# Kernel optimization log

Measured on AMD Instinct MI355X. Metric: run time of the kernel, lower is better.

Reference implementation:

```python
import jax, jax.numpy as jnp
import numpy as np

NEG_SLOPE = 0.2  # PyG GATConv default leaky_relu slope


def _gat_conv(x, src, dst, W, a_src, a_dst, b, num_nodes):
    # Linear transform: [N, F_out]
    h = x @ W
    # Per-node attention halves (heads=1): [N]
    alpha_s = h @ a_src
    alpha_d = h @ a_dst
    # Per-edge raw score for edge j->i: a_src.h_j + a_dst.h_i
    e = jax.nn.leaky_relu(alpha_s[src] + alpha_d[dst], NEG_SLOPE)
    # Softmax over edges grouped by destination node (numerically stable)
    m = jax.ops.segment_max(e, dst, num_segments=num_nodes)
    ex = jnp.exp(e - m[dst])
    denom = jax.ops.segment_sum(ex, dst, num_segments=num_nodes)
    coef = ex / denom[dst]
    # Attention-weighted aggregation of source features into destinations
    out = jax.ops.segment_sum(h[src] * coef[:, None], dst, num_segments=num_nodes)
    return out + b


def setup_inputs() -> dict:
    key = jax.random.key(0)
    ks = jax.random.split(key, 12)
    N, F_in, F_hid, F_out, E = 100000, 128, 64, 40, 1600000
    x = jax.random.normal(ks[0], (N, F_in), dtype=jnp.float32)
    edge_index = jax.random.randint(ks[1], (2, E), 0, N, dtype=jnp.int64)
    g = lambda k, shape, fan: jax.random.normal(k, shape, dtype=jnp.float32) * (1.0 / np.sqrt(fan))
    return {
        "x": x,
        "edge_index": edge_index,
        "W1": g(ks[2], (F_in, F_hid), F_in),
        "a_src1": g(ks[3], (F_hid,), F_hid),
        "a_dst1": g(ks[4], (F_hid,), F_hid),
        "b1": jnp.zeros((F_hid,), dtype=jnp.float32),
        "W2": g(ks[5], (F_hid, F_out), F_hid),
        "a_src2": g(ks[6], (F_out,), F_out),
        "a_dst2": g(ks[7], (F_out,), F_out),
        "b2": jnp.zeros((F_out,), dtype=jnp.float32),
    }


def reference(x, edge_index, W1, a_src1, a_dst1, b1, W2, a_src2, a_dst2, b2):
    N = x.shape[0]
    # PyG GATConv adds self loops by default
    loops = jnp.arange(N, dtype=edge_index.dtype)
    src = jnp.concatenate([edge_index[0], loops])
    dst = jnp.concatenate([edge_index[1], loops])
    h = _gat_conv(x, src, dst, W1, a_src1, a_dst1, b1, N)
    h = jax.nn.relu(h)
    # dropout p=0.5 is inactive in eval mode
    h = _gat_conv(h, src, dst, W2, a_src2, a_dst2, b2, N)
    return jax.nn.log_softmax(h, axis=-1)
```

## Files before the change

### kernel.cpp

```cpp
#include <hip/hip_runtime.h>
#include <math.h>


constexpr int F_IN = 128;
constexpr int F_H  = 64;
constexpr int F_O  = 40;
constexpr int NBMAX = 512;
constexpr int CHUNK = 8192;

__device__ __forceinline__ unsigned f2bf(float f) {
    unsigned u = __float_as_uint(f);
    return (u + 0x7FFFu + ((u >> 16) & 1u)) >> 16;
}
__device__ __forceinline__ float bflo(unsigned u) { return __uint_as_float(u << 16); }
__device__ __forceinline__ float bfhi(unsigned u) { return __uint_as_float(u & 0xFFFF0000u); }


__global__ __launch_bounds__(256) void k_binA(const int* __restrict__ dsts,
                                              int* __restrict__ bcnt,
                                              int E, int Et, int NB) {
    __shared__ int hist[NBMAX];
    for (int i = threadIdx.x; i < NB; i += 256) hist[i] = 0;
    __syncthreads();
    int e0 = blockIdx.x * 2048;
#pragma unroll
    for (int it = 0; it < 8; ++it) {
        int e = e0 + it * 256 + threadIdx.x;
        if (e < Et) {
            int d = (e < E) ? dsts[e] : (e - E);
            atomicAdd(&hist[d >> 8], 1);
        }
    }
    __syncthreads();
    for (int i = threadIdx.x; i < NB; i += 256) {
        int c = hist[i];
        if (c) atomicAdd(&bcnt[i], c);
    }
}

__global__ __launch_bounds__(NBMAX) void k_binB(const int* __restrict__ bcnt,
                                                int* __restrict__ bbase,
                                                int* __restrict__ bcur,
                                                int* __restrict__ rp,
                                                int NB, int N, int Et) {
    __shared__ int sc[NBMAX];
    int t = threadIdx.x;
    int v = (t < NB) ? bcnt[t] : 0;
    sc[t] = v; __syncthreads();
    int x = v;
    for (int o = 1; o < NBMAX; o <<= 1) {
        int y = (t >= o) ? sc[t - o] : 0;
        __syncthreads();
        x += y;
        sc[t] = x;
        __syncthreads();
    }
    if (t < NB) { int b = x - v; bbase[t] = b; bcur[t] = b; }
    if (t == 0) rp[N] = Et;
}

__global__ __launch_bounds__(256) void k_binC(const int* __restrict__ srcs,
                                              const int* __restrict__ dsts,
                                              int* __restrict__ bcur,
                                              unsigned* __restrict__ binned,
                                              int E, int Et, int NB) {
    __shared__ int hist[NBMAX];
    __shared__ int gbase[NBMAX];
    __shared__ int lcnt[NBMAX];
    int t = threadIdx.x;
    for (int i = t; i < NB; i += 256) hist[i] = 0;
    __syncthreads();
    int e0 = blockIdx.x * CHUNK;
#pragma unroll 4
    for (int it = 0; it < CHUNK / 256; ++it) {
        int e = e0 + it * 256 + t;
        if (e < Et) {
            int d = (e < E) ? dsts[e] : (e - E);
            atomicAdd(&hist[d >> 8], 1);
        }
    }
    __syncthreads();
    for (int i = t; i < NB; i += 256) {
        int c = hist[i];
        gbase[i] = c ? atomicAdd(&bcur[i], c) : 0;
        lcnt[i] = 0;
    }
    __syncthreads();
#pragma unroll 4
    for (int it = 0; it < CHUNK / 256; ++it) {
        int e = e0 + it * 256 + t;
        if (e < Et) {
            int s, d;
            if (e < E) { s = srcs[e]; d = dsts[e]; } else { s = e - E; d = s; }
            int b = d >> 8;
            int p = atomicAdd(&lcnt[b], 1);
            binned[gbase[b] + p] = (unsigned)s | ((unsigned)(d & 255) << 24);
        }
    }
}

__global__ __launch_bounds__(256) void k_binD(const unsigned* __restrict__ binned,
                                              const int* __restrict__ bbase,
                                              const int* __restrict__ bcur,
                                              int* __restrict__ rp,
                                              int* __restrict__ csr, int N) {
    __shared__ int hist[256];
    __shared__ int sc[256];
    __shared__ int lcnt[256];
    int b = blockIdx.x, t = threadIdx.x;
    int base = bbase[b], end = bcur[b];
    hist[t] = 0; __syncthreads();
    for (int j = base + t; j < end; j += 256)
        atomicAdd(&hist[binned[j] >> 24], 1);
    __syncthreads();
    int v = hist[t];
    sc[t] = v; __syncthreads();
    int x = v;
    for (int o = 1; o < 256; o <<= 1) {
        int y = (t >= o) ? sc[t - o] : 0;
        __syncthreads();
        x += y;
        sc[t] = x;
        __syncthreads();
    }
    int pref = x - v;
    int g = (b << 8) + t;
    if (g < N) rp[g] = base + pref;
    sc[t] = pref;
    lcnt[t] = 0;
    __syncthreads();
    for (int j = base + t; j < end; j += 256) {
        unsigned w = binned[j];
        int v2 = (int)(w >> 24);
        int s = (int)(w & 0xFFFFFFu);
        int p = atomicAdd(&lcnt[v2], 1);
        csr[base + sc[v2] + p] = s;
    }
}


__global__ __launch_bounds__(256) void k_gemm1(const float* __restrict__ x,
                                               const float* __restrict__ W,
                                               const float* __restrict__ avs,
                                               const float* __restrict__ avd,
                                               unsigned short* __restrict__ h,
                                               float* __restrict__ as,
                                               float* __restrict__ ad, int N) {
    __shared__ __align__(16) float Ws[F_IN * F_H];
    for (int i = threadIdx.x; i < F_IN * F_H; i += 256) Ws[i] = W[i];
    __syncthreads();
    int t = threadIdx.x;
    int r0 = blockIdx.x * 64 + (t >> 4) * 4;
    int c0 = (t & 15) * 4;
    if (r0 >= N) return;
    const float* xp = x + (size_t)r0 * F_IN;
    float acc[4][4] = {};
    for (int k4 = 0; k4 < F_IN / 4; ++k4) {
        int kb = k4 * 4;
        float4 w0 = *(const float4*)&Ws[(kb + 0) * F_H + c0];
        float4 w1 = *(const float4*)&Ws[(kb + 1) * F_H + c0];
        float4 w2 = *(const float4*)&Ws[(kb + 2) * F_H + c0];
        float4 w3 = *(const float4*)&Ws[(kb + 3) * F_H + c0];
#pragma unroll
        for (int r = 0; r < 4; ++r) {
            float4 xv = *(const float4*)&xp[(size_t)r * F_IN + kb];
            acc[r][0] += xv.x * w0.x + xv.y * w1.x + xv.z * w2.x + xv.w * w3.x;
            acc[r][1] += xv.x * w0.y + xv.y * w1.y + xv.z * w2.y + xv.w * w3.y;
            acc[r][2] += xv.x * w0.z + xv.y * w1.z + xv.z * w2.z + xv.w * w3.z;
            acc[r][3] += xv.x * w0.w + xv.y * w1.w + xv.z * w2.w + xv.w * w3.w;
        }
    }
    float4 avs4 = *(const float4*)&avs[c0];
    float4 avd4 = *(const float4*)&avd[c0];
#pragma unroll
    for (int r = 0; r < 4; ++r) {
        unsigned lo = f2bf(acc[r][0]) | (f2bf(acc[r][1]) << 16);
        unsigned hi = f2bf(acc[r][2]) | (f2bf(acc[r][3]) << 16);
        ((uint2*)h)[((size_t)(r0 + r) * F_H + c0) >> 2] = make_uint2(lo, hi);
        float ps = acc[r][0] * avs4.x + acc[r][1] * avs4.y + acc[r][2] * avs4.z + acc[r][3] * avs4.w;
        float pd = acc[r][0] * avd4.x + acc[r][1] * avd4.y + acc[r][2] * avd4.z + acc[r][3] * avd4.w;
#pragma unroll
        for (int o = 8; o; o >>= 1) {
            ps += __shfl_xor(ps, o, 16);
            pd += __shfl_xor(pd, o, 16);
        }
        if ((t & 15) == 0) { as[r0 + r] = ps; ad[r0 + r] = pd; }
    }
}


__global__ __launch_bounds__(256) void k_gemm2(const float* __restrict__ xin,
                                               const float* __restrict__ W,
                                               const float* __restrict__ avs,
                                               const float* __restrict__ avd,
                                               unsigned short* __restrict__ h,
                                               float* __restrict__ as,
                                               float* __restrict__ ad, int N) {
    __shared__ __align__(16) float Ws[F_H * F_O];
    for (int i = threadIdx.x; i < F_H * F_O; i += 256) Ws[i] = W[i];
    __syncthreads();
    int t = threadIdx.x;
    int r0 = blockIdx.x * 64 + (t >> 3) * 2;
    int l = t & 7;
    if (r0 >= N) return;
    const float4* xa = (const float4*)(xin + (size_t)r0 * F_H);
    const float4* xb = (const float4*)(xin + (size_t)(r0 + 1) * F_H);
    float acca[5] = {}, accb[5] = {};
#pragma unroll
    for (int k4 = 0; k4 < F_H / 4; ++k4) {
        float4 xva = xa[k4];
        float4 xvb = xb[k4];
        int kb = k4 * 4;
#pragma unroll
        for (int kk = 0; kk < 4; ++kk) {
            const float* wr = &Ws[(kb + kk) * F_O + l];
            float w0 = wr[0], w1 = wr[8], w2 = wr[16], w3 = wr[24], w4 = wr[32];
            float xs = (&xva.x)[kk];
            acca[0] += xs * w0; acca[1] += xs * w1; acca[2] += xs * w2;
            acca[3] += xs * w3; acca[4] += xs * w4;
            float ys = (&xvb.x)[kk];
            accb[0] += ys * w0; accb[1] += ys * w1; accb[2] += ys * w2;
            accb[3] += ys * w3; accb[4] += ys * w4;
        }
    }
    float psa = 0.f, pda = 0.f, psb = 0.f, pdb = 0.f;
    unsigned short* ra = h + (size_t)r0 * F_H;
    unsigned short* rb = h + (size_t)(r0 + 1) * F_H;
#pragma unroll
    for (int cc = 0; cc < 5; ++cc) {
        int c = l + 8 * cc;
        ra[c] = (unsigned short)f2bf(acca[cc]);
        rb[c] = (unsigned short)f2bf(accb[cc]);
        float vs = avs[c], vd = avd[c];
        psa += acca[cc] * vs; pda += acca[cc] * vd;
        psb += accb[cc] * vs; pdb += accb[cc] * vd;
    }
#pragma unroll
    for (int pp = 0; pp < 3; ++pp) {
        int c = 40 + l * 3 + pp;
        ra[c] = 0; rb[c] = 0;
    }
#pragma unroll
    for (int o = 4; o; o >>= 1) {
        psa += __shfl_xor(psa, o, 8);
        pda += __shfl_xor(pda, o, 8);
        psb += __shfl_xor(psb, o, 8);
        pdb += __shfl_xor(pdb, o, 8);
    }
    if (l == 0) { as[r0] = psa; ad[r0] = pda; as[r0 + 1] = psb; ad[r0 + 1] = pdb; }
}


template <int FOUT, bool RELU, bool LOGSM>
__global__ __launch_bounds__(256) void k_agg(const int* __restrict__ rp,
                                             const int* __restrict__ csr,
                                             const float* __restrict__ as,
                                             const float* __restrict__ ad,
                                             const uint4* __restrict__ h4,
                                             const float* __restrict__ bias,
                                             float* __restrict__ out, int N) {
    constexpr int DMAX = 256;
    __shared__ uint2 wsb[4][DMAX];
    int wslot = threadIdx.x >> 6;
    int lane = threadIdx.x & 63;
    int i = (blockIdx.x * 256 + threadIdx.x) >> 6;
    if (i >= N) return;
    int start = rp[i], end = rp[i + 1];
    int deg = end - start;
    int dm = min(deg, DMAX);
    int dmR = (dm + 31) & ~31;
    float adi = ad[i];
    float sacc = 0.f;
    for (int idx = lane; idx < dm; idx += 64) {
        int srcn = csr[start + idx];
        float e = as[srcn] + adi;
        e = (e > 0.f) ? e : 0.2f * e;
        float w = __expf(e);
        sacc += w;
        wsb[wslot][idx] = make_uint2(__float_as_uint(w), (unsigned)srcn);
    }
    {
        int idx = dm + lane;
        if (idx < dmR) wsb[wslot][idx] = make_uint2(0u, (unsigned)i);
    }

    int grp = lane >> 3, c = lane & 7;
    float acc[8] = {}, acc2[8] = {};

    for (int jb = start + dm; jb < end; jb += 8) {
        int j = jb + grp;
        bool valid = (j < end);
        int srcn = valid ? csr[j] : i;
        float e = as[srcn] + adi;
        e = (e > 0.f) ? e : 0.2f * e;
        float w = valid ? __expf(e) : 0.f;
        if (c == 0) sacc += w;
        uint4 hv = h4[(size_t)srcn * 8 + c];
        acc[0] += w * bflo(hv.x); acc[1] += w * bfhi(hv.x);
        acc[2] += w * bflo(hv.y); acc[3] += w * bfhi(hv.y);
        acc[4] += w * bflo(hv.z); acc[5] += w * bfhi(hv.z);
        acc[6] += w * bflo(hv.w); acc[7] += w * bfhi(hv.w);
    }

    for (int off = 0; off < dmR; off += 32) {
        uint2 t0 = wsb[wslot][off + grp];
        uint2 t1 = wsb[wslot][off + 8 + grp];
        uint2 t2 = wsb[wslot][off + 16 + grp];
        uint2 t3 = wsb[wslot][off + 24 + grp];
        uint4 hv0 = h4[(size_t)t0.y * 8 + c];
        uint4 hv1 = h4[(size_t)t1.y * 8 + c];
        uint4 hv2 = h4[(size_t)t2.y * 8 + c];
        uint4 hv3 = h4[(size_t)t3.y * 8 + c];
        float w0 = __uint_as_float(t0.x);
        float w1 = __uint_as_float(t1.x);
        float w2 = __uint_as_float(t2.x);
        float w3 = __uint_as_float(t3.x);
        acc[0] += w0 * bflo(hv0.x); acc[1] += w0 * bfhi(hv0.x);
        acc[2] += w0 * bflo(hv0.y); acc[3] += w0 * bfhi(hv0.y);
        acc[4] += w0 * bflo(hv0.z); acc[5] += w0 * bfhi(hv0.z);
        acc[6] += w0 * bflo(hv0.w); acc[7] += w0 * bfhi(hv0.w);
        acc2[0] += w1 * bflo(hv1.x); acc2[1] += w1 * bfhi(hv1.x);
        acc2[2] += w1 * bflo(hv1.y); acc2[3] += w1 * bfhi(hv1.y);
        acc2[4] += w1 * bflo(hv1.z); acc2[5] += w1 * bfhi(hv1.z);
        acc2[6] += w1 * bflo(hv1.w); acc2[7] += w1 * bfhi(hv1.w);
        acc[0] += w2 * bflo(hv2.x); acc[1] += w2 * bfhi(hv2.x);
        acc[2] += w2 * bflo(hv2.y); acc[3] += w2 * bfhi(hv2.y);
        acc[4] += w2 * bflo(hv2.z); acc[5] += w2 * bfhi(hv2.z);
        acc[6] += w2 * bflo(hv2.w); acc[7] += w2 * bfhi(hv2.w);
        acc2[0] += w3 * bflo(hv3.x); acc2[1] += w3 * bfhi(hv3.x);
        acc2[2] += w3 * bflo(hv3.y); acc2[3] += w3 * bfhi(hv3.y);
        acc2[4] += w3 * bflo(hv3.z); acc2[5] += w3 * bfhi(hv3.z);
        acc2[6] += w3 * bflo(hv3.w); acc2[7] += w3 * bfhi(hv3.w);
    }
#pragma unroll
    for (int k = 0; k < 8; ++k) acc[k] += acc2[k];
#pragma unroll
    for (int o = 8; o <= 32; o <<= 1)
#pragma unroll
        for (int k = 0; k < 8; ++k) acc[k] += __shfl_xor(acc[k], o);
#pragma unroll
    for (int o = 32; o; o >>= 1) sacc += __shfl_xor(sacc, o);
    float inv = 1.f / sacc;

    if (!LOGSM) {
        if (lane < 8) {
            float r[8];
#pragma unroll
            for (int k = 0; k < 8; ++k) {
                r[k] = acc[k] * inv + bias[8 * lane + k];
                if (RELU) r[k] = fmaxf(r[k], 0.f);
            }
            float4* op = (float4*)(out + (size_t)i * FOUT + 8 * lane);
            op[0] = make_float4(r[0], r[1], r[2], r[3]);
            op[1] = make_float4(r[4], r[5], r[6], r[7]);
        }
    } else {
        constexpr int VC = FOUT / 8;
        bool act = (lane < VC);
        float v[8];
#pragma unroll
        for (int k = 0; k < 8; ++k)
            v[k] = act ? (acc[k] * inv + bias[8 * lane + k]) : -INFINITY;
        float mx = v[0];
#pragma unroll
        for (int k = 1; k < 8; ++k) mx = fmaxf(mx, v[k]);
#pragma unroll
        for (int o = 1; o <= 4; o <<= 1) mx = fmaxf(mx, __shfl_xor(mx, o));
        float es = 0.f;
        if (act) {
#pragma unroll
            for (int k = 0; k < 8; ++k) es += __expf(v[k] - mx);
        }
#pragma unroll
        for (int o = 1; o <= 4; o <<= 1) es += __shfl_xor(es, o);
        if (act) {
            float lse = mx + __logf(es);
            float4* op = (float4*)(out + (size_t)i * FOUT + 8 * lane);
            op[0] = make_float4(v[0] - lse, v[1] - lse, v[2] - lse, v[3] - lse);
            op[1] = make_float4(v[4] - lse, v[5] - lse, v[6] - lse, v[7] - lse);
        }
    }
}


extern "C" void kernel_launch(void* const* d_in, const int* in_sizes, int n_in,
                              void* d_out, int out_size, void* d_ws, size_t ws_size,
                              hipStream_t stream) {
    const float* x   = (const float*)d_in[0];
    const int* edges = (const int*)d_in[1];
    const float* W1  = (const float*)d_in[2];
    const float* av_s1 = (const float*)d_in[3];
    const float* av_d1 = (const float*)d_in[4];
    const float* b1  = (const float*)d_in[5];
    const float* W2  = (const float*)d_in[6];
    const float* av_s2 = (const float*)d_in[7];
    const float* av_d2 = (const float*)d_in[8];
    const float* b2  = (const float*)d_in[9];
    float* out = (float*)d_out;

    const int N  = in_sizes[0] / F_IN;
    const int E  = in_sizes[1] / 2;
    const int Et = E + N;
    const int NB = (N + 255) >> 8;

    char* p = (char*)d_ws;
    auto alloc = [&](size_t bytes) {
        char* q = p;
        p += (bytes + 255) & ~(size_t)255;
        return (void*)q;
    };
    unsigned short* h1 = (unsigned short*)alloc((size_t)N * F_H * 2);
    float* out1   = (float*)alloc((size_t)N * F_H * 4);
    float* as1    = (float*)alloc((size_t)N * 4);
    float* ad1    = (float*)alloc((size_t)N * 4);
    float* as2    = (float*)alloc((size_t)N * 4);
    float* ad2    = (float*)alloc((size_t)N * 4);
    int* rp       = (int*)alloc((size_t)(N + 1) * 4);
    int* bcnt     = (int*)alloc(NBMAX * 4);
    int* bbase    = (int*)alloc(NBMAX * 4);
    int* bcur     = (int*)alloc(NBMAX * 4);
    unsigned* binned = (unsigned*)alloc((size_t)Et * 4);
    int* csr      = (int*)alloc((size_t)Et * 4);
    (void)n_in; (void)out_size; (void)ws_size;

    const int* srcs = edges;
    const int* dsts = edges + E;

    hipMemsetAsync(bcnt, 0, NBMAX * 4, stream);

    k_binA<<<(Et + 2047) / 2048, 256, 0, stream>>>(dsts, bcnt, E, Et, NB);
    k_binB<<<1, NBMAX, 0, stream>>>(bcnt, bbase, bcur, rp, NB, N, Et);
    k_binC<<<(Et + CHUNK - 1) / CHUNK, 256, 0, stream>>>(srcs, dsts, bcur, binned, E, Et, NB);
    k_binD<<<NB, 256, 0, stream>>>(binned, bbase, bcur, rp, csr, N);

    k_gemm1<<<(N + 63) / 64, 256, 0, stream>>>(x, W1, av_s1, av_d1, h1, as1, ad1, N);
    int gAgg = (N + 3) / 4;
    k_agg<F_H, true, false><<<gAgg, 256, 0, stream>>>(rp, csr, as1, ad1,
                                                      (const uint4*)h1, b1, out1, N);
    k_gemm2<<<(N + 63) / 64, 256, 0, stream>>>(out1, W2, av_s2, av_d2, h1, as2, ad2, N);
    k_agg<F_O, false, true><<<gAgg, 256, 0, stream>>>(rp, csr, as2, ad2,
                                                      (const uint4*)h1, b2, out, N);
}
```

Before: 338.2 us.

## Aggregate with 8 lanes per node and packed fp16 dot2 accumulation

The aggregation kernel moves from one 64-lane wavefront per destination node to one 8-lane group per node, so 32 nodes share a block and the cross-lane reductions go away. Intermediate features are stored as fp16 instead of bf16 so that two edges can be accumulated per instruction with packed fdot2, with edge weights also rounded to fp16. This targets idle lanes on low-degree nodes (about 17 edges on average) and the ALU cost of unpacking. The trade-offs are less parallelism per high-degree node, a serial tail loop for degrees above 64, and a risk of fp16 range or precision loss in the attention weights and features.

```diff
diff --git a/kernel.cpp b/kernel.cpp
--- a/kernel.cpp
+++ b/kernel.cpp
@@ -8,12 +8,28 @@
 constexpr int NBMAX = 512;
 constexpr int CHUNK = 8192;
 
-__device__ __forceinline__ unsigned f2bf(float f) {
-    unsigned u = __float_as_uint(f);
-    return (u + 0x7FFFu + ((u >> 16) & 1u)) >> 16;
-}
-__device__ __forceinline__ float bflo(unsigned u) { return __uint_as_float(u << 16); }
-__device__ __forceinline__ float bfhi(unsigned u) { return __uint_as_float(u & 0xFFFF0000u); }
+using h2 = decltype(__builtin_amdgcn_cvt_pkrtz(0.f, 0.f));
+
+__device__ __forceinline__ h2 u2h(unsigned u) { return __builtin_bit_cast(h2, u); }
+__device__ __forceinline__ unsigned h2u(h2 h) { return __builtin_bit_cast(unsigned, h); }
+
+__device__ __forceinline__ float fdot2f(h2 a, h2 b, float c) {
+#if __has_builtin(__builtin_amdgcn_fdot2)
+    return __builtin_amdgcn_fdot2(a, b, c, false);
+#else
+    return c + (float)a.x * (float)b.x + (float)a.y * (float)b.y;
+#endif
+}
+__device__ __forceinline__ h2 pklo(unsigned a, unsigned b) {
+    return u2h(__builtin_amdgcn_perm(a, b, 0x05040100u));
+}
+__device__ __forceinline__ h2 pkhi(unsigned a, unsigned b) {
+    return u2h(__builtin_amdgcn_perm(a, b, 0x07060302u));
+}
+__device__ __forceinline__ unsigned short f2h(float f) {
+    _Float16 x = (_Float16)f;
+    return __builtin_bit_cast(unsigned short, x);
+}
 
 
 __global__ __launch_bounds__(256) void k_binA(const int* __restrict__ dsts,
@@ -174,8 +190,8 @@
     float4 avd4 = *(const float4*)&avd[c0];
 #pragma unroll
     for (int r = 0; r < 4; ++r) {
-        unsigned lo = f2bf(acc[r][0]) | (f2bf(acc[r][1]) << 16);
-        unsigned hi = f2bf(acc[r][2]) | (f2bf(acc[r][3]) << 16);
+        unsigned lo = h2u(__builtin_amdgcn_cvt_pkrtz(acc[r][0], acc[r][1]));
+        unsigned hi = h2u(__builtin_amdgcn_cvt_pkrtz(acc[r][2], acc[r][3]));
         ((uint2*)h)[((size_t)(r0 + r) * F_H + c0) >> 2] = make_uint2(lo, hi);
         float ps = acc[r][0] * avs4.x + acc[r][1] * avs4.y + acc[r][2] * avs4.z + acc[r][3] * avs4.w;
         float pd = acc[r][0] * avd4.x + acc[r][1] * avd4.y + acc[r][2] * avd4.z + acc[r][3] * avd4.w;
@@ -229,8 +245,8 @@
 #pragma unroll
     for (int cc = 0; cc < 5; ++cc) {
         int c = l + 8 * cc;
-        ra[c] = (unsigned short)f2bf(acca[cc]);
-        rb[c] = (unsigned short)f2bf(accb[cc]);
+        ra[c] = f2h(acca[cc]);
+        rb[c] = f2h(accb[cc]);
         float vs = avs[c], vd = avd[c];
         psa += acca[cc] * vs; pda += acca[cc] * vd;
         psb += accb[cc] * vs; pdb += accb[cc] * vd;
@@ -259,108 +275,87 @@
                                              const uint4* __restrict__ h4,
                                              const float* __restrict__ bias,
                                              float* __restrict__ out, int N) {
-    constexpr int DMAX = 256;
-    __shared__ uint2 wsb[4][DMAX];
-    int wslot = threadIdx.x >> 6;
-    int lane = threadIdx.x & 63;
-    int i = (blockIdx.x * 256 + threadIdx.x) >> 6;
+    constexpr int CAP = 64;
+    __shared__ __align__(16) uint2 wsb[4][8][CAP + 2];
+    const int w = threadIdx.x >> 6;
+    const int g = (threadIdx.x >> 3) & 7;
+    const int c = threadIdx.x & 7;
+    const int i = blockIdx.x * 32 + (threadIdx.x >> 3);
     if (i >= N) return;
-    int start = rp[i], end = rp[i + 1];
-    int deg = end - start;
-    int dm = min(deg, DMAX);
-    int dmR = (dm + 31) & ~31;
-    float adi = ad[i];
-    float sacc = 0.f;
-    for (int idx = lane; idx < dm; idx += 64) {
+    const int start = rp[i], end = rp[i + 1];
+    const int deg = end - start;
+    const int dm = min(deg, CAP);
+    const float adi = ad[i];
+
+    for (int idx = c; idx < dm; idx += 8) {
         int srcn = csr[start + idx];
         float e = as[srcn] + adi;
-        e = (e > 0.f) ? e : 0.2f * e;
-        float w = __expf(e);
-        sacc += w;
-        wsb[wslot][idx] = make_uint2(__float_as_uint(w), (unsigned)srcn);
-    }
-    {
-        int idx = dm + lane;
-        if (idx < dmR) wsb[wslot][idx] = make_uint2(0u, (unsigned)i);
-    }
-
-    int grp = lane >> 3, c = lane & 7;
-    float acc[8] = {}, acc2[8] = {};
-
-    for (int jb = start + dm; jb < end; jb += 8) {
-        int j = jb + grp;
-        bool valid = (j < end);
-        int srcn = valid ? csr[j] : i;
+        e = fmaxf(e, 0.2f * e);
+        wsb[w][g][idx] = make_uint2(__float_as_uint(__expf(e)), (unsigned)srcn);
+    }
+    if (c == 0 && (dm & 1))
+        wsb[w][g][dm] = make_uint2(0u, (unsigned)i);
+
+    const uint4* pw = (const uint4*)wsb[w][g];
+    float acc[8] = {};
+    float sacc = 0.f;
+    const int npair = (dm + 1) >> 1;
+    for (int p = 0; p < npair; ++p) {
+        uint4 t = pw[p];
+        float w0 = __uint_as_float(t.x), w1 = __uint_as_float(t.z);
+        sacc += w0 + w1;
+        uint4 hv0 = h4[((unsigned)t.y << 3) + c];
+        uint4 hv1 = h4[((unsigned)t.w << 3) + c];
+        h2 wp = __builtin_amdgcn_cvt_pkrtz(w0, w1);
+        acc[0] = fdot2f(wp, pklo(hv1.x, hv0.x), acc[0]);
+        acc[1] = fdot2f(wp, pkhi(hv1.x, hv0.x), acc[1]);
+        acc[2] = fdot2f(wp, pklo(hv1.y, hv0.y), acc[2]);
+        acc[3] = fdot2f(wp, pkhi(hv1.y, hv0.y), acc[3]);
+        acc[4] = fdot2f(wp, pklo(hv1.z, hv0.z), acc[4]);
+        acc[5] = fdot2f(wp, pkhi(hv1.z, hv0.z), acc[5]);
+        acc[6] = fdot2f(wp, pklo(hv1.w, hv0.w), acc[6]);
+        acc[7] = fdot2f(wp, pkhi(hv1.w, hv0.w), acc[7]);
+    }
+
+    for (int j = start + dm; j < end; ++j) {
+        int srcn = csr[j];
         float e = as[srcn] + adi;
-        e = (e > 0.f) ? e : 0.2f * e;
-        float w = valid ? __expf(e) : 0.f;
-        if (c == 0) sacc += w;
-        uint4 hv = h4[(size_t)srcn * 8 + c];
-        acc[0] += w * bflo(hv.x); acc[1] += w * bfhi(hv.x);
-        acc[2] += w * bflo(hv.y); acc[3] += w * bfhi(hv.y);
-        acc[4] += w * bflo(hv.z); acc[5] += w * bfhi(hv.z);
-        acc[6] += w * bflo(hv.w); acc[7] += w * bfhi(hv.w);
-    }
-
-    for (int off = 0; off < dmR; off += 32) {
-        uint2 t0 = wsb[wslot][off + grp];
-        uint2 t1 = wsb[wslot][off + 8 + grp];
-        uint2 t2 = wsb[wslot][off + 16 + grp];
-        uint2 t3 = wsb[wslot][off + 24 + grp];
-        uint4 hv0 = h4[(size_t)t0.y * 8 + c];
-        uint4 hv1 = h4[(size_t)t1.y * 8 + c];
-        uint4 hv2 = h4[(size_t)t2.y * 8 + c];
-        uint4 hv3 = h4[(size_t)t3.y * 8 + c];
-        float w0 = __uint_as_float(t0.x);
-        float w1 = __uint_as_float(t1.x);
-        float w2 = __uint_as_float(t2.x);
-        float w3 = __uint_as_float(t3.x);
-        acc[0] += w0 * bflo(hv0.x); acc[1] += w0 * bfhi(hv0.x);
-        acc[2] += w0 * bflo(hv0.y); acc[3] += w0 * bfhi(hv0.y);
-        acc[4] += w0 * bflo(hv0.z); acc[5] += w0 * bfhi(hv0.z);
-        acc[6] += w0 * bflo(hv0.w); acc[7] += w0 * bfhi(hv0.w);
-        acc2[0] += w1 * bflo(hv1.x); acc2[1] += w1 * bfhi(hv1.x);
-        acc2[2] += w1 * bflo(hv1.y); acc2[3] += w1 * bfhi(hv1.y);
-        acc2[4] += w1 * bflo(hv1.z); acc2[5] += w1 * bfhi(hv1.z);
-        acc2[6] += w1 * bflo(hv1.w); acc2[7] += w1 * bfhi(hv1.w);
-        acc[0] += w2 * bflo(hv2.x); acc[1] += w2 * bfhi(hv2.x);
-        acc[2] += w2 * bflo(hv2.y); acc[3] += w2 * bfhi(hv2.y);
-        acc[4] += w2 * bflo(hv2.z); acc[5] += w2 * bfhi(hv2.z);
-        acc[6] += w2 * bflo(hv2.w); acc[7] += w2 * bfhi(hv2.w);
-        acc2[0] += w3 * bflo(hv3.x); acc2[1] += w3 * bfhi(hv3.x);
-        acc2[2] += w3 * bflo(hv3.y); acc2[3] += w3 * bfhi(hv3.y);
-        acc2[4] += w3 * bflo(hv3.z); acc2[5] += w3 * bfhi(hv3.z);
-        acc2[6] += w3 * bflo(hv3.w); acc2[7] += w3 * bfhi(hv3.w);
-    }
-#pragma unroll
-    for (int k = 0; k < 8; ++k) acc[k] += acc2[k];
-#pragma unroll
-    for (int o = 8; o <= 32; o <<= 1)
-#pragma unroll
-        for (int k = 0; k < 8; ++k) acc[k] += __shfl_xor(acc[k], o);
-#pragma unroll
-    for (int o = 32; o; o >>= 1) sacc += __shfl_xor(sacc, o);
+        e = fmaxf(e, 0.2f * e);
+        float wv = __expf(e);
+        sacc += wv;
+        uint4 hv = h4[((unsigned)srcn << 3) + c];
+        h2 wp = __builtin_amdgcn_cvt_pkrtz(wv, 0.f);
+        acc[0] = fdot2f(wp, pklo(hv.x, hv.x), acc[0]);
+        acc[1] = fdot2f(wp, pkhi(hv.x, hv.x), acc[1]);
+        acc[2] = fdot2f(wp, pklo(hv.y, hv.y), acc[2]);
+        acc[3] = fdot2f(wp, pkhi(hv.y, hv.y), acc[3]);
+        acc[4] = fdot2f(wp, pklo(hv.z, hv.z), acc[4]);
+        acc[5] = fdot2f(wp, pkhi(hv.z, hv.z), acc[5]);
+        acc[6] = fdot2f(wp, pklo(hv.w, hv.w), acc[6]);
+        acc[7] = fdot2f(wp, pkhi(hv.w, hv.w), acc[7]);
+    }
+
     float inv = 1.f / sacc;
 
     if (!LOGSM) {
-        if (lane < 8) {
-            float r[8];
-#pragma unroll
-            for (int k = 0; k < 8; ++k) {
-                r[k] = acc[k] * inv + bias[8 * lane + k];
-                if (RELU) r[k] = fmaxf(r[k], 0.f);
-            }
-            float4* op = (float4*)(out + (size_t)i * FOUT + 8 * lane);
-            op[0] = make_float4(r[0], r[1], r[2], r[3]);
-            op[1] = make_float4(r[4], r[5], r[6], r[7]);
-        }
+        float r[8];
+#pragma unroll
+        for (int k = 0; k < 8; ++k) {
+            r[k] = fmaf(acc[k], inv, bias[8 * c + k]);
+            if (RELU) r[k] = fmaxf(r[k], 0.f);
+        }
+        float4* op = (float4*)(out + (size_t)i * FOUT + 8 * c);
+        op[0] = make_float4(r[0], r[1], r[2], r[3]);
+        op[1] = make_float4(r[4], r[5], r[6], r[7]);
     } else {
         constexpr int VC = FOUT / 8;
-        bool act = (lane < VC);
+        bool act = (c < VC);
         float v[8];
 #pragma unroll
-        for (int k = 0; k < 8; ++k)
-            v[k] = act ? (acc[k] * inv + bias[8 * lane + k]) : -INFINITY;
+        for (int k = 0; k < 8; ++k) {
+            float bv = bias[act ? 8 * c + k : 0];
+            v[k] = act ? fmaf(acc[k], inv, bv) : -INFINITY;
+        }
         float mx = v[0];
 #pragma unroll
         for (int k = 1; k < 8; ++k) mx = fmaxf(mx, v[k]);
@@ -375,7 +370,7 @@
         for (int o = 1; o <= 4; o <<= 1) es += __shfl_xor(es, o);
         if (act) {
             float lse = mx + __logf(es);
-            float4* op = (float4*)(out + (size_t)i * FOUT + 8 * lane);
+            float4* op = (float4*)(out + (size_t)i * FOUT + 8 * c);
             op[0] = make_float4(v[0] - lse, v[1] - lse, v[2] - lse, v[3] - lse);
             op[1] = make_float4(v[4] - lse, v[5] - lse, v[6] - lse, v[7] - lse);
         }
@@ -434,7 +429,7 @@
     k_binD<<<NB, 256, 0, stream>>>(binned, bbase, bcur, rp, csr, N);
 
     k_gemm1<<<(N + 63) / 64, 256, 0, stream>>>(x, W1, av_s1, av_d1, h1, as1, ad1, N);
-    int gAgg = (N + 3) / 4;
+    int gAgg = (N + 31) / 32;
     k_agg<F_H, true, false><<<gAgg, 256, 0, stream>>>(rp, csr, as1, ad1,
                                                       (const uint4*)h1, b1, out1, N);
     k_gemm2<<<(N + 63) / 64, 256, 0, stream>>>(out1, W2, av_s2, av_d2, h1, as2, ad2, N);
```

Result: faster. 307.9 us (-8.9%).
